# Kernel tuning notes

Measured on AMD Instinct MI355X. Metric: run time of the kernel, lower is better.

The kernel has to match this reference:

```python
import jax, jax.numpy as jnp
import numpy as np

B, S, D_MODEL = 1, 2048, 4096
N_HEADS, N_KV_HEADS = 32, 8
HEAD_DIM = D_MODEL // N_HEADS  # 128
N_REP = N_HEADS // N_KV_HEADS  # 4
ROPE_THETA = 500000.0
NEG_INF = -1e9


def setup_inputs() -> dict:
    key = jax.random.key(0)
    ks = jax.random.split(key, 6)
    std = 0.02 * (2 * 32) ** (-0.5)
    x = jax.random.normal(ks[0], (B, S, D_MODEL), dtype=jnp.float32)
    wq = jax.random.normal(ks[1], (N_HEADS * HEAD_DIM, D_MODEL), dtype=jnp.float32) * std
    wk = jax.random.normal(ks[2], (N_KV_HEADS * HEAD_DIM, D_MODEL), dtype=jnp.float32) * std
    wv = jax.random.normal(ks[3], (N_KV_HEADS * HEAD_DIM, D_MODEL), dtype=jnp.float32) * std
    wo = jax.random.normal(ks[4], (D_MODEL, N_HEADS * HEAD_DIM), dtype=jnp.float32) * std
    cache_k = jnp.zeros((B, S, N_KV_HEADS, HEAD_DIM), dtype=jnp.float32)
    cache_v = jnp.zeros((B, S, N_KV_HEADS, HEAD_DIM), dtype=jnp.float32)
    # RoPE tables: freqs_cis[t, j] = exp(i * t * theta^(-2j/head_dim)), j < head_dim/2
    inv_freq = 1.0 / (ROPE_THETA ** (jnp.arange(0, HEAD_DIM, 2, dtype=jnp.float32) / HEAD_DIM))
    t = jnp.arange(S, dtype=jnp.float32)
    ang = jnp.outer(t, inv_freq)  # [S, HEAD_DIM/2]
    freqs_cos = jnp.cos(ang)
    freqs_sin = jnp.sin(ang)
    # causal additive mask [1, 1, S, S]
    mask = jnp.triu(jnp.full((S, S), NEG_INF, dtype=jnp.float32), k=1)[None, None]
    return {"x": x, "wq": wq, "wk": wk, "wv": wv, "wo": wo,
            "cache_k": cache_k, "cache_v": cache_v,
            "freqs_cos": freqs_cos, "freqs_sin": freqs_sin,
            "mask": mask, "start_pos": 0}


def _apply_rope(x, cos, sin):
    # x: [B, S, H, D]; cos/sin: [S, D/2]; pairs (x[2j], x[2j+1]) form complex numbers
    b, s, h, d = x.shape
    x2 = x.astype(jnp.float32).reshape(b, s, h, d // 2, 2)
    xr, xi = x2[..., 0], x2[..., 1]
    c = cos[None, :, None, :]
    sn = sin[None, :, None, :]
    out_r = xr * c - xi * sn
    out_i = xr * sn + xi * c
    return jnp.stack([out_r, out_i], axis=-1).reshape(b, s, h, d)


def reference(x, wq, wk, wv, wo, cache_k, cache_v, freqs_cos, freqs_sin, mask, start_pos):
    bsz, seq_len, _ = x.shape
    xq = (x @ wq.T).reshape(bsz, seq_len, N_HEADS, HEAD_DIM)
    xk = (x @ wk.T).reshape(bsz, seq_len, N_KV_HEADS, HEAD_DIM)
    xv = (x @ wv.T).reshape(bsz, seq_len, N_KV_HEADS, HEAD_DIM)
    xq = _apply_rope(xq, freqs_cos, freqs_sin)
    xk = _apply_rope(xk, freqs_cos, freqs_sin)
    # KV-cache update then read back the valid prefix
    cache_k = jax.lax.dynamic_update_slice(cache_k, xk, (0, start_pos, 0, 0))
    cache_v = jax.lax.dynamic_update_slice(cache_v, xv, (0, start_pos, 0, 0))
    keys = cache_k[:, : start_pos + seq_len]      # [B, K, KVH, D]
    values = cache_v[:, : start_pos + seq_len]
    # repeat_kv: expand kv heads to match query heads
    keys = jnp.repeat(keys, N_REP, axis=2)        # [B, K, H, D]
    values = jnp.repeat(values, N_REP, axis=2)
    q = xq.transpose(0, 2, 1, 3)                  # [B, H, S, D]
    k = keys.transpose(0, 2, 1, 3)                # [B, H, K, D]
    v = values.transpose(0, 2, 1, 3)
    scores = jnp.einsum('bhqd,bhkd->bhqk', q, k) / jnp.float32(np.sqrt(HEAD_DIM))
    scores = scores + mask
    probs = jax.nn.softmax(scores.astype(jnp.float32), axis=-1).astype(q.dtype)
    out = jnp.einsum('bhqk,bhkd->bhqd', probs, v)           # [B, H, S, D]
    out = out.transpose(0, 2, 1, 3).reshape(bsz, seq_len, -1)
    return out @ wo.T
```

## Files before the change

### kernel.cpp

```cpp
#include <hip/hip_runtime.h>
#include <cstdint>
#include <cstddef>

typedef __attribute__((ext_vector_type(8))) short  short8;
typedef __attribute__((ext_vector_type(4))) float  floatx4;
typedef __attribute__((ext_vector_type(4))) unsigned short ushort4v;

__device__ __forceinline__ unsigned short f2b(float f) {
  unsigned u = __builtin_bit_cast(unsigned, f);
  u = u + 0x7fffu + ((u >> 16) & 1u);
  return (unsigned short)(u >> 16);
}
__device__ __forceinline__ float b2f(unsigned short h) {
  unsigned u = ((unsigned)h) << 16;
  return __builtin_bit_cast(float, u);
}

__device__ __forceinline__ void gld_lds16(const void* g, void* l) {
  __builtin_amdgcn_global_load_lds(
      (const __attribute__((address_space(1))) unsigned int*)g,
      (__attribute__((address_space(3))) unsigned int*)l,
      16, 0, 0);
}

__global__ void __launch_bounds__(256) f2b_kernel(const float* __restrict__ in,
                                                  unsigned short* __restrict__ out,
                                                  int n4) {
  int i = blockIdx.x * 256 + threadIdx.x;
  if (i >= n4) return;
  floatx4 v = ((const floatx4*)in)[i];
  ushort4v o;
  o[0] = f2b(v[0]); o[1] = f2b(v[1]); o[2] = f2b(v[2]); o[3] = f2b(v[3]);
  ((ushort4v*)out)[i] = o;
}

template <int MODE>
__global__ void __launch_bounds__(256) gemm_bt(const unsigned short* __restrict__ A,
                                               const unsigned short* __restrict__ B,
                                               float* __restrict__ Cf,
                                               unsigned short* __restrict__ Cb,
                                               int M, int N, int K,
                                               const float* __restrict__ fc,
                                               const float* __restrict__ fs) {
  __shared__ __align__(16) unsigned short As[4096];
  __shared__ __align__(16) unsigned short Bs[4096];
  const int m0 = blockIdx.x * 128;
  const int n0 = blockIdx.y * 128;
  const int tid  = threadIdx.x;
  const int wave = tid >> 6, lane = tid & 63;
  const int quad = lane >> 4, l15 = lane & 15;
  const int wm = ((wave >> 1) & 1) * 64;
  const int wn = (wave & 1) * 64;

  floatx4 acc[4][4] = {};

  const int lr = lane >> 2, sj = lane & 3;
  const unsigned short* pa[2];
  const unsigned short* pb[2];
  unsigned short *la[2], *lb[2];
#pragma unroll
  for (int t = 0; t < 2; ++t) {
    const int i = wave * 2 + t;
    const int r = i * 16 + lr;
    const int o = (sj - (r >> 1)) & 3;
    pa[t] = A + (size_t)(m0 + r) * K + o * 8;
    pb[t] = B + (size_t)(n0 + r) * K + o * 8;
    la[t] = &As[i * 512];
    lb[t] = &Bs[i * 512];
  }

  for (int kt = 0; kt < K; kt += 32) {
    gld_lds16(pa[0] + kt, la[0]);
    gld_lds16(pa[1] + kt, la[1]);
    gld_lds16(pb[0] + kt, lb[0]);
    gld_lds16(pb[1] + kt, lb[1]);
    __syncthreads();

    short8 af[4], bfr[4];
#pragma unroll
    for (int t = 0; t < 4; ++t) {
      const int rA = wm + t * 16 + l15;
      const int ja = (quad + (rA >> 1)) & 3;
      af[t] = *(const short8*)&As[rA * 32 + ja * 8];
      const int rB = wn + t * 16 + l15;
      const int jb = (quad + (rB >> 1)) & 3;
      bfr[t] = *(const short8*)&Bs[rB * 32 + jb * 8];
    }
#pragma unroll
    for (int tm = 0; tm < 4; ++tm)
#pragma unroll
      for (int tn = 0; tn < 4; ++tn)
        acc[tm][tn] = __builtin_amdgcn_mfma_f32_16x16x32_bf16(af[tm], bfr[tn], acc[tm][tn], 0, 0, 0);
    __syncthreads();
  }

#pragma unroll
  for (int tm = 0; tm < 4; ++tm) {
#pragma unroll
    for (int tn = 0; tn < 4; ++tn) {
      const int colb = n0 + wn + tn * 16;
      const int col  = colb + l15;
      const bool rope = (MODE == 2) && (colb < 5120);
      const int p = (col & 127) >> 1;
      const float sgn = (l15 & 1) ? 1.f : -1.f;
#pragma unroll
      for (int r = 0; r < 4; ++r) {
        const int row = m0 + wm + tm * 16 + quad * 4 + r;
        float v = acc[tm][tn][r];
        if (rope) {
          const float partner = __shfl_xor(v, 1);
          const float c  = fc[row * 64 + p];
          const float sn = fs[row * 64 + p];
          v = v * c + partner * sn * sgn;
        }
        if (MODE == 1) Cf[(size_t)row * N + col] = v;
        else           Cb[(size_t)row * N + col] = f2b(v);
      }
    }
  }
}

__global__ void __launch_bounds__(256) transpose_bf16(const unsigned short* __restrict__ in,
                                                      unsigned short* __restrict__ out,
                                                      int R, int C, int in_stride) {
  __shared__ __align__(16) unsigned short tile[64][72];
  const int br = blockIdx.y * 64;
  const int bc = blockIdx.x * 64;
  const int tid = threadIdx.x;
  const int lr = tid >> 3;
  const int lc = (tid & 7) * 8;
#pragma unroll
  for (int it = 0; it < 2; ++it) {
    const int r = it * 32 + lr;
    *(short8*)&tile[r][lc] = *(const short8*)(in + (size_t)(br + r) * in_stride + bc + lc);
  }
  __syncthreads();
#pragma unroll
  for (int it = 0; it < 2; ++it) {
    const int c = it * 32 + lr;
    short8 v;
#pragma unroll
    for (int j = 0; j < 8; ++j) v[j] = (short)tile[lc + j][c];
    *(short8*)(out + (size_t)(bc + c) * R + br + lc) = v;
  }
}

#define SL2E 0.1275500406721347f

__global__ void __launch_bounds__(256) flash_attn(const unsigned short* __restrict__ Q,
                                                  const unsigned short* __restrict__ Kp,
                                                  const unsigned short* __restrict__ Vt,
                                                  unsigned short* __restrict__ O) {
  constexpr int QS = 6144;
  const int bx  = blockIdx.x;
  const int h   = blockIdx.y;
  const int kvh = h >> 2;
  const int tid = threadIdx.x;
  const int wave = tid >> 6, lane = tid & 63;
  const int quad = lane >> 4, l15 = lane & 15;

  __shared__ __align__(16) unsigned short Ks[2][8192];
  __shared__ __align__(16) unsigned short Vs[2][8192];
  __shared__ __align__(16) unsigned short Ps[4][16 * 76];
  unsigned short* Pw = Ps[wave];

  const int i0 = wave * 4;
  const unsigned short* kbase = Kp + kvh * 128;
  const unsigned short* vbase[4];
  int vslot_sc[4];
#pragma unroll
  for (int ii = 0; ii < 4; ++ii) {
    const int i = i0 + ii;
    const int slot = i * 64 + lane;
    const int sc = slot >> 7, d = slot & 127;
    vbase[ii] = Vt + (size_t)(kvh * 128 + d) * 2048;
    vslot_sc[ii] = sc * 8;
  }

  for (int seg = 0; seg < 2; ++seg) {
    const int qt  = seg ? (31 - bx) : bx;
    const int q0  = qt * 64;
    const int qra = q0 + wave * 16;
    const int n   = qt + 1;

    short8 aq[4];
#pragma unroll
    for (int ks = 0; ks < 4; ++ks)
      aq[ks] = *(const short8*)(Q + (size_t)(qra + l15) * QS + h * 128 + ks * 32 + quad * 8);

    floatx4 oacc[8] = {};
    float mrow[4], lrow[4];
#pragma unroll
    for (int r = 0; r < 4; ++r) { mrow[r] = -1e30f; lrow[r] = 0.f; }

    {
      const int cc = 0;
#pragma unroll
      for (int ii = 0; ii < 4; ++ii) {
        const int i = i0 + ii;
        gld_lds16(kbase + (size_t)(cc + lane) * QS + i * 8, &Ks[0][i * 512]);
        gld_lds16(vbase[ii] + cc + vslot_sc[ii], &Vs[0][i * 512]);
      }
    }

    for (int j = 0; j < n; ++j) {
      __syncthreads();
      if (j + 1 < n) {
        const int cc = (j + 1) * 64;
        const int nb = (j + 1) & 1;
#pragma unroll
        for (int ii = 0; ii < 4; ++ii) {
          const int i = i0 + ii;
          gld_lds16(kbase + (size_t)(cc + lane) * QS + i * 8, &Ks[nb][i * 512]);
          gld_lds16(vbase[ii] + cc + vslot_sc[ii], &Vs[nb][i * 512]);
        }
      }
      const unsigned short* kb = Ks[j & 1];
      const unsigned short* vb = Vs[j & 1];
      const int c0 = j * 64;

      floatx4 sacc[4] = {};
#pragma unroll
      for (int ks = 0; ks < 4; ++ks) {
#pragma unroll
        for (int tn = 0; tn < 4; ++tn) {
          short8 bk = *(const short8*)&kb[((ks * 4 + quad) * 64 + tn * 16 + l15) * 8];
          sacc[tn] = __builtin_amdgcn_mfma_f32_16x16x32_bf16(aq[ks], bk, sacc[tn], 0, 0, 0);
        }
      }

      const bool needmask = (c0 + 63 > qra);
#pragma unroll
      for (int r = 0; r < 4; ++r) {
        const int rowg = qra + quad * 4 + r;
        float t0 = sacc[0][r] * SL2E, t1 = sacc[1][r] * SL2E;
        float t2 = sacc[2][r] * SL2E, t3 = sacc[3][r] * SL2E;
        if (needmask) {
          t0 = (c0 +  0 + l15 <= rowg) ? t0 : -1e30f;
          t1 = (c0 + 16 + l15 <= rowg) ? t1 : -1e30f;
          t2 = (c0 + 32 + l15 <= rowg) ? t2 : -1e30f;
          t3 = (c0 + 48 + l15 <= rowg) ? t3 : -1e30f;
        }
        float mx = fmaxf(fmaxf(t0, t1), fmaxf(t2, t3));
#pragma unroll
        for (int off = 1; off < 16; off <<= 1)
          mx = fmaxf(mx, __shfl_xor(mx, off, 16));
        const float mold = mrow[r];
        const float mn   = fmaxf(mold, mx);
        const float alpha = exp2f(mold - mn);
        float p0 = exp2f(t0 - mn), p1 = exp2f(t1 - mn);
        float p2 = exp2f(t2 - mn), p3 = exp2f(t3 - mn);
        sacc[0][r] = p0; sacc[1][r] = p1; sacc[2][r] = p2; sacc[3][r] = p3;
        float lsum = (p0 + p1) + (p2 + p3);
#pragma unroll
        for (int off = 1; off < 16; off <<= 1)
          lsum += __shfl_xor(lsum, off, 16);
        mrow[r] = mn;
        lrow[r] = lrow[r] * alpha + lsum;
#pragma unroll
        for (int tn = 0; tn < 8; ++tn) oacc[tn][r] *= alpha;
      }

#pragma unroll
      for (int tn = 0; tn < 4; ++tn)
#pragma unroll
        for (int r = 0; r < 4; ++r)
          Pw[(quad * 4 + r) * 76 + tn * 16 + l15] = f2b(sacc[tn][r]);

      short8 ap[2];
#pragma unroll
      for (int k2 = 0; k2 < 2; ++k2)
        ap[k2] = *(const short8*)&Pw[l15 * 76 + k2 * 32 + quad * 8];
#pragma unroll
      for (int k2 = 0; k2 < 2; ++k2) {
#pragma unroll
        for (int tn = 0; tn < 8; ++tn) {
          short8 bv = *(const short8*)&vb[((k2 * 4 + quad) * 128 + tn * 16 + l15) * 8];
          oacc[tn] = __builtin_amdgcn_mfma_f32_16x16x32_bf16(ap[k2], bv, oacc[tn], 0, 0, 0);
        }
      }
    }

#pragma unroll
    for (int r = 0; r < 4; ++r) {
      const float inv = 1.f / lrow[r];
      const int rowg = qra + quad * 4 + r;
#pragma unroll
      for (int tn = 0; tn < 8; ++tn)
        O[(size_t)rowg * 4096 + h * 128 + tn * 16 + l15] = f2b(oacc[tn][r] * inv);
    }
    __syncthreads();
  }
}

extern "C" void kernel_launch(void* const* d_in, const int* in_sizes, int n_in,
                              void* d_out, int out_size, void* d_ws, size_t ws_size,
                              hipStream_t stream) {
  const float* x  = (const float*)d_in[0];
  const float* wq = (const float*)d_in[1];
  const float* wk = (const float*)d_in[2];
  const float* wv = (const float*)d_in[3];
  const float* wo = (const float*)d_in[4];
  const float* fc = (const float*)d_in[7];
  const float* fs = (const float*)d_in[8];
  float* out = (float*)d_out;

  char* ws = (char*)d_ws;
  unsigned short* xb    = (unsigned short*)(ws + 0);
  unsigned short* wqkvb = (unsigned short*)(ws + 16777216);
  unsigned short* wob   = (unsigned short*)(ws + 67108864);
  unsigned short* qkv   = (unsigned short*)(ws + 100663296);
  unsigned short* vt    = (unsigned short*)(ws + 125829120);
  unsigned short* ob    = (unsigned short*)(ws + 130023424);
  unsigned short* wkb = wqkvb + (size_t)4096 * 4096;
  unsigned short* wvb = wkb + (size_t)1024 * 4096;

  f2b_kernel<<<8192,  256, 0, stream>>>(x,  xb,    2097152);
  f2b_kernel<<<16384, 256, 0, stream>>>(wq, wqkvb, 4194304);
  f2b_kernel<<<4096,  256, 0, stream>>>(wk, wkb,   1048576);
  f2b_kernel<<<4096,  256, 0, stream>>>(wv, wvb,   1048576);
  f2b_kernel<<<16384, 256, 0, stream>>>(wo, wob,   4194304);

  gemm_bt<2><<<dim3(16, 48), 256, 0, stream>>>(xb, wqkvb, nullptr, qkv, 2048, 6144, 4096, fc, fs);

  transpose_bf16<<<dim3(16, 32), 256, 0, stream>>>(qkv + 5120, vt, 2048, 1024, 6144);

  flash_attn<<<dim3(16, 32), 256, 0, stream>>>(qkv, qkv + 4096, vt, ob);

  gemm_bt<1><<<dim3(16, 32), 256, 0, stream>>>(ob, wob, out, nullptr, 2048, 4096, 4096, nullptr, nullptr);
}
```

Measured before the change: 648.9 us.

## Double-buffer GEMM A tiles, load B from global into registers, fuse casts

The GEMM now double-buffers the A tile in LDS, prefetching the next k-slice while computing the current one, which removes one barrier per iteration. B fragments are read straight from global memory into registers with one-iteration lookahead instead of being staged through LDS. The five fp32-to-bf16 conversion launches are merged into a single kernel to cut launch overhead. Reading B directly from global gives up LDS reuse of B across the two M-waves, so global traffic for B doubles and depends on L2 hit rates.

```diff
diff --git a/kernel.cpp b/kernel.cpp
--- a/kernel.cpp
+++ b/kernel.cpp
@@ -23,15 +23,28 @@
       16, 0, 0);
 }
 
-__global__ void __launch_bounds__(256) f2b_kernel(const float* __restrict__ in,
-                                                  unsigned short* __restrict__ out,
-                                                  int n4) {
+__global__ void __launch_bounds__(256) f2b_multi(const float* __restrict__ x,
+                                                 const float* __restrict__ wq,
+                                                 const float* __restrict__ wk,
+                                                 const float* __restrict__ wv,
+                                                 const float* __restrict__ wo,
+                                                 unsigned short* __restrict__ xb,
+                                                 unsigned short* __restrict__ wqb,
+                                                 unsigned short* __restrict__ wkb,
+                                                 unsigned short* __restrict__ wvb,
+                                                 unsigned short* __restrict__ wob) {
   int i = blockIdx.x * 256 + threadIdx.x;
-  if (i >= n4) return;
-  floatx4 v = ((const floatx4*)in)[i];
+  const float* in; unsigned short* out; int off;
+  if      (i <  2097152) { in = x;  out = xb;  off = 0;       }
+  else if (i <  6291456) { in = wq; out = wqb; off = 2097152; }
+  else if (i <  7340032) { in = wk; out = wkb; off = 6291456; }
+  else if (i <  8388608) { in = wv; out = wvb; off = 7340032; }
+  else                   { in = wo; out = wob; off = 8388608; }
+  const int k = i - off;
+  floatx4 v = ((const floatx4*)in)[k];
   ushort4v o;
   o[0] = f2b(v[0]); o[1] = f2b(v[1]); o[2] = f2b(v[2]); o[3] = f2b(v[3]);
-  ((ushort4v*)out)[i] = o;
+  ((ushort4v*)out)[k] = o;
 }
 
 template <int MODE>
@@ -42,8 +55,7 @@
                                                int M, int N, int K,
                                                const float* __restrict__ fc,
                                                const float* __restrict__ fs) {
-  __shared__ __align__(16) unsigned short As[4096];
-  __shared__ __align__(16) unsigned short Bs[4096];
+  __shared__ __align__(16) unsigned short As[2][4096];
   const int m0 = blockIdx.x * 128;
   const int n0 = blockIdx.y * 128;
   const int tid  = threadIdx.x;
@@ -56,42 +68,54 @@
 
   const int lr = lane >> 2, sj = lane & 3;
   const unsigned short* pa[2];
-  const unsigned short* pb[2];
-  unsigned short *la[2], *lb[2];
+  int laoff[2];
 #pragma unroll
   for (int t = 0; t < 2; ++t) {
     const int i = wave * 2 + t;
     const int r = i * 16 + lr;
     const int o = (sj - (r >> 1)) & 3;
     pa[t] = A + (size_t)(m0 + r) * K + o * 8;
-    pb[t] = B + (size_t)(n0 + r) * K + o * 8;
-    la[t] = &As[i * 512];
-    lb[t] = &Bs[i * 512];
-  }
-
-  for (int kt = 0; kt < K; kt += 32) {
-    gld_lds16(pa[0] + kt, la[0]);
-    gld_lds16(pa[1] + kt, la[1]);
-    gld_lds16(pb[0] + kt, lb[0]);
-    gld_lds16(pb[1] + kt, lb[1]);
+    laoff[t] = i * 512;
+  }
+
+  const unsigned short* pb[4];
+#pragma unroll
+  for (int tn = 0; tn < 4; ++tn)
+    pb[tn] = B + (size_t)(n0 + wn + tn * 16 + l15) * K + quad * 8;
+
+  gld_lds16(pa[0], &As[0][laoff[0]]);
+  gld_lds16(pa[1], &As[0][laoff[1]]);
+  short8 bcur[4];
+#pragma unroll
+  for (int tn = 0; tn < 4; ++tn) bcur[tn] = *(const short8*)pb[tn];
+
+  const int niter = K >> 5;
+  for (int j = 0; j < niter; ++j) {
     __syncthreads();
-
-    short8 af[4], bfr[4];
+    const int ktn = (j + 1) << 5;
+    if (j + 1 < niter) {
+      gld_lds16(pa[0] + ktn, &As[(j + 1) & 1][laoff[0]]);
+      gld_lds16(pa[1] + ktn, &As[(j + 1) & 1][laoff[1]]);
+    }
+    short8 af[4];
 #pragma unroll
     for (int t = 0; t < 4; ++t) {
       const int rA = wm + t * 16 + l15;
       const int ja = (quad + (rA >> 1)) & 3;
-      af[t] = *(const short8*)&As[rA * 32 + ja * 8];
-      const int rB = wn + t * 16 + l15;
-      const int jb = (quad + (rB >> 1)) & 3;
-      bfr[t] = *(const short8*)&Bs[rB * 32 + jb * 8];
+      af[t] = *(const short8*)&As[j & 1][rA * 32 + ja * 8];
+    }
+    short8 bnext[4];
+    if (j + 1 < niter) {
+#pragma unroll
+      for (int tn = 0; tn < 4; ++tn) bnext[tn] = *(const short8*)(pb[tn] + ktn);
     }
 #pragma unroll
     for (int tm = 0; tm < 4; ++tm)
 #pragma unroll
       for (int tn = 0; tn < 4; ++tn)
-        acc[tm][tn] = __builtin_amdgcn_mfma_f32_16x16x32_bf16(af[tm], bfr[tn], acc[tm][tn], 0, 0, 0);
-    __syncthreads();
+        acc[tm][tn] = __builtin_amdgcn_mfma_f32_16x16x32_bf16(af[tm], bcur[tn], acc[tm][tn], 0, 0, 0);
+#pragma unroll
+    for (int tn = 0; tn < 4; ++tn) bcur[tn] = bnext[tn];
   }
 
 #pragma unroll
@@ -315,11 +339,7 @@
   unsigned short* wkb = wqkvb + (size_t)4096 * 4096;
   unsigned short* wvb = wkb + (size_t)1024 * 4096;
 
-  f2b_kernel<<<8192,  256, 0, stream>>>(x,  xb,    2097152);
-  f2b_kernel<<<16384, 256, 0, stream>>>(wq, wqkvb, 4194304);
-  f2b_kernel<<<4096,  256, 0, stream>>>(wk, wkb,   1048576);
-  f2b_kernel<<<4096,  256, 0, stream>>>(wv, wvb,   1048576);
-  f2b_kernel<<<16384, 256, 0, stream>>>(wo, wob,   4194304);
+  f2b_multi<<<49152, 256, 0, stream>>>(x, wq, wk, wv, wo, xb, wqkvb, wkb, wvb, wob);
 
   gemm_bt<2><<<dim3(16, 48), 256, 0, stream>>>(xb, wqkvb, nullptr, qkv, 2048, 6144, 4096, fc, fs);
 
```

Result: slower. 734.7 us (+13.2%).
